# Performance work log

Hardware: AMD Instinct MI355X
Metric: run time of the kernel (lower is better)

The kernel has to match this reference:

```python
import jax, jax.numpy as jnp
import numpy as np

N_NODES = 50000
N_EDGES = 600000
N_GRAPHS = 64
HID = 128
NLAYERS = 4
IN_DIM = 5
NCLS = 5
EPS = 1e-5


def setup_inputs() -> dict:
    key = jax.random.key(0)
    ks = jax.random.split(key, 16)
    x = jax.random.normal(ks[0], (N_NODES, IN_DIM), dtype=jnp.float32)
    edge_index = jax.random.randint(ks[1], (2, N_EDGES), 0, N_NODES, dtype=jnp.int64)
    batch = jnp.sort(jax.random.randint(ks[2], (N_NODES,), 0, N_GRAPHS, dtype=jnp.int64))
    s = 0.05
    Wp = jax.random.normal(ks[3], (IN_DIM, HID), jnp.float32) * s
    bp = jnp.zeros((HID,), jnp.float32)
    Wg = jax.random.normal(ks[4], (NLAYERS, HID, HID), jnp.float32) * s
    bg = jnp.zeros((NLAYERS, HID), jnp.float32)
    gamma = jnp.ones((NLAYERS, HID), jnp.float32)
    beta = jnp.zeros((NLAYERS, HID), jnp.float32)
    W1 = jax.random.normal(ks[5], (2 * HID, HID), jnp.float32) * s
    b1 = jnp.zeros((HID,), jnp.float32)
    W2 = jax.random.normal(ks[6], (HID, HID // 2), jnp.float32) * s
    b2 = jnp.zeros((HID // 2,), jnp.float32)
    W3 = jax.random.normal(ks[7], (HID // 2, NCLS), jnp.float32) * s
    b3 = jnp.zeros((NCLS,), jnp.float32)
    return {"x": x, "edge_index": edge_index, "batch": batch, "Wp": Wp, "bp": bp,
            "Wg": Wg, "bg": bg, "gamma": gamma, "beta": beta,
            "W1": W1, "b1": b1, "W2": W2, "b2": b2, "W3": W3, "b3": b3}


def reference(x, edge_index, batch, Wp, bp, Wg, bg, gamma, beta, W1, b1, W2, b2, W3, b3):
    N = x.shape[0]
    # GCN with added self-loops and symmetric normalization (PyG GCNConv defaults)
    loop = jnp.arange(N)
    src = jnp.concatenate([edge_index[0], loop])
    dst = jnp.concatenate([edge_index[1], loop])
    deg = jax.ops.segment_sum(jnp.ones_like(dst, dtype=x.dtype), dst, num_segments=N)
    dinv = jax.lax.rsqrt(deg)  # deg >= 1 thanks to self-loops
    norm = dinv[src] * dinv[dst]  # [E+N]
    h = x @ Wp + bp  # [N, HID]
    for i in range(NLAYERS):
        m = h @ Wg[i]
        agg = jax.ops.segment_sum(m[src] * norm[:, None], dst, num_segments=N) + bg[i]
        # BatchNorm1d (training-mode stats over nodes)
        mu = jnp.mean(agg, axis=0)
        var = jnp.var(agg, axis=0)
        h = gamma[i] * (agg - mu) * jax.lax.rsqrt(var + EPS) + beta[i]
        h = jax.nn.relu(h)  # dropout is identity in eval mode
    # mean_max global pooling per graph
    cnt = jax.ops.segment_sum(jnp.ones((N,), h.dtype), batch, num_segments=N_GRAPHS)
    x_mean = jax.ops.segment_sum(h, batch, num_segments=N_GRAPHS) / jnp.maximum(cnt, 1.0)[:, None]
    x_max = jax.ops.segment_max(h, batch, num_segments=N_GRAPHS)
    x_max = jnp.where(jnp.isfinite(x_max), x_max, 0.0)
    pooled = jnp.concatenate([x_mean, x_max], axis=1)  # [B, 2*HID]
    h1 = jax.nn.relu(pooled @ W1 + b1)
    h2 = jax.nn.relu(h1 @ W2 + b2)
    return h2 @ W3 + b3  # [B, num_classes]
```

## Files before the change

### kernel.cpp

```cpp
#include <hip/hip_runtime.h>
#include <hip/hip_bf16.h>

#define N_NODES 50000
#define N_EDGES 600000
#define N_GRAPHS 64
#define HID 128
#define NLAYERS 4
#define IN_DIM 5
#define NCLS 5
#define EPS 1e-5f
#define SCAN_BLK ((N_NODES + 511) / 512)
#define POOL_CHUNKS 16
#define BSLOT 64
#define WS 136

typedef __attribute__((ext_vector_type(8))) short s16x8;
typedef __attribute__((ext_vector_type(4))) float f32x4;

__device__ __forceinline__ unsigned short f2bf(float x) {
    unsigned u = __float_as_uint(x);
    unsigned r = (u + 0x7fffu + ((u >> 16) & 1u)) >> 16;
    return (unsigned short)r;
}
__device__ __forceinline__ float2 bfpair(unsigned u) {
    float2 r;
    r.x = __uint_as_float(u << 16);
    r.y = __uint_as_float(u & 0xffff0000u);
    return r;
}
__device__ __forceinline__ float bf2f(unsigned short s) {
    return __uint_as_float(((unsigned)s) << 16);
}


__global__ void k_count(const int* __restrict__ dst, int* __restrict__ cnt) {
    int i = blockIdx.x * blockDim.x + threadIdx.x;
    if (i < N_EDGES) atomicAdd(&cnt[dst[i]], 1);
}

__global__ void k_scan1(const int* __restrict__ cnt, int* __restrict__ rp, int* __restrict__ bsum) {
    __shared__ int s[512];
    int t = threadIdx.x;
    int i = blockIdx.x * 512 + t;
    int v = (i < N_NODES) ? cnt[i] : 0;
    s[t] = v;
    __syncthreads();
    for (int off = 1; off < 512; off <<= 1) {
        int x = (t >= off) ? s[t - off] : 0;
        __syncthreads();
        s[t] += x;
        __syncthreads();
    }
    if (i < N_NODES) rp[i + 1] = s[t];
    if (t == 511) bsum[blockIdx.x] = s[511];
}

__global__ void k_scan2g(int* __restrict__ bsum, const int* __restrict__ batch,
                         int* __restrict__ gstart) {
    if (blockIdx.x == 0) {
        __shared__ int s[128];
        int t = threadIdx.x;
        int v = (t < SCAN_BLK) ? bsum[t] : 0;
        s[t] = v;
        __syncthreads();
        for (int off = 1; off < 128; off <<= 1) {
            int x = (t >= off) ? s[t - off] : 0;
            __syncthreads();
            s[t] += x;
            __syncthreads();
        }
        if (t < SCAN_BLK) bsum[t] = s[t] - v;
    } else {
        int t = threadIdx.x;
        if (t <= N_GRAPHS) {
            int lo = 0, hi = N_NODES;
            while (lo < hi) {
                int mid = (lo + hi) >> 1;
                if (batch[mid] < t) lo = mid + 1; else hi = mid;
            }
            gstart[t] = lo;
        }
    }
}

__global__ void k_scan3d(int* __restrict__ rp, const int* __restrict__ bsum,
                         const int* __restrict__ cnt, float* __restrict__ dinv) {
    int i = blockIdx.x * 512 + threadIdx.x;
    if (i < N_NODES) {
        rp[i + 1] += bsum[blockIdx.x];
        dinv[i] = rsqrtf((float)(cnt[i] + 1));
    }
    if (i == 0) rp[0] = 0;
}

__global__ void k_fill(const int* __restrict__ src, const int* __restrict__ dst,
                       const int* __restrict__ rp, int* __restrict__ cursor,
                       int2* __restrict__ cw, const float* __restrict__ dinv) {
    int e = blockIdx.x * blockDim.x + threadIdx.x;
    if (e < N_EDGES) {
        int d = dst[e];
        int pos = atomicAdd(&cursor[d], 1);
        int s = src[e];
        int2 p;
        p.x = s;
        p.y = __float_as_int(dinv[s]);
        cw[rp[d] + pos] = p;
    }
}


__global__ void k_wconv(const float* __restrict__ Wg, unsigned short* __restrict__ WtG) {
    int idx = blockIdx.x * 256 + threadIdx.x;
    if (idx < NLAYERS * HID * HID) {
        int l = idx >> 14;
        int r = idx & 16383;
        int n = r >> 7, k = r & 127;
        WtG[idx] = f2bf(Wg[l * HID * HID + k * HID + n]);
    }
}


__global__ __launch_bounds__(256) void k_gemmM(const unsigned short* __restrict__ Abf,
                                               const float* __restrict__ x,
                                               const float* __restrict__ Wp,
                                               const float* __restrict__ bp,
                                               const unsigned short* __restrict__ WtG,
                                               unsigned short* __restrict__ Bm,
                                               const float* __restrict__ psum,
                                               const float* __restrict__ psq,
                                               const float* __restrict__ gamma,
                                               const float* __restrict__ beta,
                                               int layer0) {
    __shared__ unsigned short Wt[HID * WS];
    __shared__ unsigned short Al[64 * WS];
    __shared__ float scl[HID], shf[HID];
    __shared__ float Wpl[IN_DIM * HID];
    __shared__ float bpl[HID];
    __shared__ float xl[64 * IN_DIM];
    int t = threadIdx.x;
    {
        const uint4* Wg4 = (const uint4*)WtG;
        for (int idx = t; idx < HID * 16; idx += 256) {
            int n = idx >> 4, c = idx & 15;
            *(uint4*)&Wt[n * WS + c * 8] = Wg4[idx];
        }
    }
    if (layer0) {
        for (int idx = t; idx < IN_DIM * HID; idx += 256) Wpl[idx] = Wp[idx];
        if (t < HID) bpl[t] = bp[t];
    } else if (t < HID) {
        float s = 0.f, s2 = 0.f;
#pragma unroll 8
        for (int b = 0; b < BSLOT; b++) {
            s += psum[b * HID + t];
            s2 += psq[b * HID + t];
        }
        const float invN = 1.f / (float)N_NODES;
        float mu = s * invN;
        float var = s2 * invN - mu * mu;
        float rs = rsqrtf(var + EPS) * gamma[t];
        scl[t] = rs;
        shf[t] = beta[t] - mu * rs;
    }
    int lane = t & 63, wv = t >> 6;
    int rbase = (wv & 1) * 32;
    int cbase = (wv >> 1) * 64;
    int mr = lane & 15, q = lane >> 4;
    const int numTiles = (N_NODES + 63) / 64;
    for (int tile = blockIdx.x; tile < numTiles; tile += gridDim.x) {
        int n0 = tile * 64;
        __syncthreads();
        if (layer0) {
            for (int idx = t; idx < 64 * IN_DIM; idx += 256) {
                int g = n0 * IN_DIM + idx;
                xl[idx] = (g < N_NODES * IN_DIM) ? x[g] : 0.f;
            }
            __syncthreads();
            for (int idx = t; idx < 64 * HID; idx += 256) {
                int n = idx >> 7, k = idx & 127;
                float acc = bpl[k];
#pragma unroll
                for (int j = 0; j < IN_DIM; j++) acc += xl[n * IN_DIM + j] * Wpl[j * HID + k];
                Al[n * WS + k] = f2bf(acc);
            }
        } else {
            const uint2* Ag = (const uint2*)(Abf + (size_t)n0 * HID);
            int limRow = min(64, N_NODES - n0);
            for (int idx = t; idx < 64 * 32; idx += 256) {
                int row = idx >> 5, c4 = idx & 31;
                uint2 u = (row < limRow) ? Ag[row * 32 + c4] : make_uint2(0u, 0u);
                float2 ab = bfpair(u.x);
                float2 cd = bfpair(u.y);
                int kf = c4 * 4;
                float4 sc = *(const float4*)&scl[kf];
                float4 sh = *(const float4*)&shf[kf];
                float v0 = fmaxf(ab.x * sc.x + sh.x, 0.f);
                float v1 = fmaxf(ab.y * sc.y + sh.y, 0.f);
                float v2 = fmaxf(cd.x * sc.z + sh.z, 0.f);
                float v3 = fmaxf(cd.y * sc.w + sh.w, 0.f);
                unsigned lo = (unsigned)f2bf(v0) | ((unsigned)f2bf(v1) << 16);
                unsigned hi = (unsigned)f2bf(v2) | ((unsigned)f2bf(v3) << 16);
                *(uint2*)&Al[row * WS + kf] = make_uint2(lo, hi);
            }
        }
        __syncthreads();
        f32x4 acc[2][4];
#pragma unroll
        for (int rt = 0; rt < 2; rt++)
#pragma unroll
            for (int ct = 0; ct < 4; ct++) acc[rt][ct] = (f32x4){0.f, 0.f, 0.f, 0.f};
#pragma unroll
        for (int kk = 0; kk < HID; kk += 32) {
            s16x8 a0 = *(const s16x8*)&Al[(rbase + mr) * WS + kk + q * 8];
            s16x8 a1 = *(const s16x8*)&Al[(rbase + 16 + mr) * WS + kk + q * 8];
#pragma unroll
            for (int ct = 0; ct < 4; ct++) {
                s16x8 b = *(const s16x8*)&Wt[(cbase + ct * 16 + mr) * WS + kk + q * 8];
                acc[0][ct] = __builtin_amdgcn_mfma_f32_16x16x32_bf16(a0, b, acc[0][ct], 0, 0, 0);
                acc[1][ct] = __builtin_amdgcn_mfma_f32_16x16x32_bf16(a1, b, acc[1][ct], 0, 0, 0);
            }
        }
#pragma unroll
        for (int rt = 0; rt < 2; rt++)
#pragma unroll
            for (int ct = 0; ct < 4; ct++)
#pragma unroll
                for (int r = 0; r < 4; r++) {
                    int node = n0 + rbase + rt * 16 + q * 4 + r;
                    if (node < N_NODES) {
                        int f = cbase + ct * 16 + mr;
                        Bm[(size_t)node * HID + f] = f2bf(acc[rt][ct][r]);
                    }
                }
    }
}


__global__ __launch_bounds__(256) void k_gather(const uint4* __restrict__ Bm4,
                                                const int* __restrict__ rp,
                                                const int2* __restrict__ cw,
                                                const float* __restrict__ dinv,
                                                const float* __restrict__ bg,
                                                unsigned short* __restrict__ Aout,
                                                float* __restrict__ psum,
                                                float* __restrict__ psq) {
    __shared__ float ls[4 * HID], lq[4 * HID];
    int wave = threadIdx.x >> 6;
    int lane = threadIdx.x & 63;
    int s = lane & 15;
    int p = lane >> 4;
    int f = s * 8;
    float ts0 = 0.f, ts1 = 0.f, ts2 = 0.f, ts3 = 0.f, ts4 = 0.f, ts5 = 0.f, ts6 = 0.f, ts7 = 0.f;
    float tq0 = 0.f, tq1 = 0.f, tq2 = 0.f, tq3 = 0.f, tq4 = 0.f, tq5 = 0.f, tq6 = 0.f, tq7 = 0.f;
#pragma unroll 1
    for (int it = 0; it < 4; it++) {
        int v = blockIdx.x * 16 + wave * 4 + it;
        int beg = rp[v], end = rp[v + 1];
        float dv = dinv[v];
        float a0 = 0.f, a1 = 0.f, a2 = 0.f, a3 = 0.f, a4 = 0.f, a5 = 0.f, a6 = 0.f, a7 = 0.f;
        if (p == 0) {
            uint4 u = Bm4[(size_t)v * 16 + s];
            float2 q0 = bfpair(u.x), q1 = bfpair(u.y), q2 = bfpair(u.z), q3 = bfpair(u.w);
            a0 = q0.x * dv; a1 = q0.y * dv; a2 = q1.x * dv; a3 = q1.y * dv;
            a4 = q2.x * dv; a5 = q2.y * dv; a6 = q3.x * dv; a7 = q3.y * dv;
        }
        int e = beg + p;
        for (; e + 4 < end; e += 8) {
            int2 pe0 = cw[e];
            int2 pe1 = cw[e + 4];
            uint4 u0 = Bm4[(size_t)pe0.x * 16 + s];
            uint4 u1 = Bm4[(size_t)pe1.x * 16 + s];
            float w0 = __int_as_float(pe0.y);
            float w1 = __int_as_float(pe1.y);
            float2 x0 = bfpair(u0.x), x1 = bfpair(u0.y), x2 = bfpair(u0.z), x3 = bfpair(u0.w);
            float2 y0 = bfpair(u1.x), y1 = bfpair(u1.y), y2 = bfpair(u1.z), y3 = bfpair(u1.w);
            a0 += x0.x * w0 + y0.x * w1;
            a1 += x0.y * w0 + y0.y * w1;
            a2 += x1.x * w0 + y1.x * w1;
            a3 += x1.y * w0 + y1.y * w1;
            a4 += x2.x * w0 + y2.x * w1;
            a5 += x2.y * w0 + y2.y * w1;
            a6 += x3.x * w0 + y3.x * w1;
            a7 += x3.y * w0 + y3.y * w1;
        }
        if (e < end) {
            int2 pe = cw[e];
            uint4 u = Bm4[(size_t)pe.x * 16 + s];
            float w = __int_as_float(pe.y);
            float2 x0 = bfpair(u.x), x1 = bfpair(u.y), x2 = bfpair(u.z), x3 = bfpair(u.w);
            a0 += x0.x * w; a1 += x0.y * w; a2 += x1.x * w; a3 += x1.y * w;
            a4 += x2.x * w; a5 += x2.y * w; a6 += x3.x * w; a7 += x3.y * w;
        }
        a0 += __shfl_xor(a0, 16); a1 += __shfl_xor(a1, 16);
        a2 += __shfl_xor(a2, 16); a3 += __shfl_xor(a3, 16);
        a4 += __shfl_xor(a4, 16); a5 += __shfl_xor(a5, 16);
        a6 += __shfl_xor(a6, 16); a7 += __shfl_xor(a7, 16);
        a0 += __shfl_xor(a0, 32); a1 += __shfl_xor(a1, 32);
        a2 += __shfl_xor(a2, 32); a3 += __shfl_xor(a3, 32);
        a4 += __shfl_xor(a4, 32); a5 += __shfl_xor(a5, 32);
        a6 += __shfl_xor(a6, 32); a7 += __shfl_xor(a7, 32);
        if (p == 0) {
            float r0 = a0 * dv + bg[f + 0];
            float r1 = a1 * dv + bg[f + 1];
            float r2 = a2 * dv + bg[f + 2];
            float r3 = a3 * dv + bg[f + 3];
            float r4 = a4 * dv + bg[f + 4];
            float r5 = a5 * dv + bg[f + 5];
            float r6 = a6 * dv + bg[f + 6];
            float r7 = a7 * dv + bg[f + 7];
            unsigned short b0 = f2bf(r0), b1 = f2bf(r1), b2 = f2bf(r2), b3 = f2bf(r3);
            unsigned short b4 = f2bf(r4), b5 = f2bf(r5), b6 = f2bf(r6), b7 = f2bf(r7);
            uint4 o;
            o.x = (unsigned)b0 | ((unsigned)b1 << 16);
            o.y = (unsigned)b2 | ((unsigned)b3 << 16);
            o.z = (unsigned)b4 | ((unsigned)b5 << 16);
            o.w = (unsigned)b6 | ((unsigned)b7 << 16);
            *(uint4*)&Aout[(size_t)v * HID + f] = o;
            float v0 = bf2f(b0), v1 = bf2f(b1), v2 = bf2f(b2), v3 = bf2f(b3);
            float v4 = bf2f(b4), v5 = bf2f(b5), v6 = bf2f(b6), v7 = bf2f(b7);
            ts0 += v0; ts1 += v1; ts2 += v2; ts3 += v3;
            ts4 += v4; ts5 += v5; ts6 += v6; ts7 += v7;
            tq0 += v0 * v0; tq1 += v1 * v1; tq2 += v2 * v2; tq3 += v3 * v3;
            tq4 += v4 * v4; tq5 += v5 * v5; tq6 += v6 * v6; tq7 += v7 * v7;
        }
    }
    if (p == 0) {
        float* lsw = &ls[wave * HID + f];
        float* lqw = &lq[wave * HID + f];
        lsw[0] = ts0; lsw[1] = ts1; lsw[2] = ts2; lsw[3] = ts3;
        lsw[4] = ts4; lsw[5] = ts5; lsw[6] = ts6; lsw[7] = ts7;
        lqw[0] = tq0; lqw[1] = tq1; lqw[2] = tq2; lqw[3] = tq3;
        lqw[4] = tq4; lqw[5] = tq5; lqw[6] = tq6; lqw[7] = tq7;
    }
    __syncthreads();
    int tt = threadIdx.x;
    if (tt < HID) {
        float ssum = ls[tt] + ls[HID + tt] + ls[2 * HID + tt] + ls[3 * HID + tt];
        float ssq = lq[tt] + lq[HID + tt] + lq[2 * HID + tt] + lq[3 * HID + tt];
        int slot = blockIdx.x & (BSLOT - 1);
        atomicAdd(&psum[slot * HID + tt], ssum);
        atomicAdd(&psq[slot * HID + tt], ssq);
    }
}


__global__ __launch_bounds__(128) void k_pool(const unsigned short* __restrict__ A,
                                              const float* __restrict__ psum,
                                              const float* __restrict__ psq,
                                              const float* __restrict__ gamma,
                                              const float* __restrict__ beta,
                                              const int* __restrict__ gstart,
                                              float* __restrict__ poolPart) {
    int g = blockIdx.x;
    int c = blockIdx.y;
    int f = threadIdx.x;
    float s = 0.f, s2 = 0.f;
#pragma unroll 8
    for (int b = 0; b < BSLOT; b++) {
        s += psum[b * HID + f];
        s2 += psq[b * HID + f];
    }
    const float invN = 1.f / (float)N_NODES;
    float mu = s * invN;
    float var = s2 * invN - mu * mu;
    float sc = rsqrtf(var + EPS) * gamma[f];
    float sh = beta[f] - mu * sc;
    int beg = gstart[g], end = gstart[g + 1];
    int len = end - beg;
    int per = (len + POOL_CHUNKS - 1) / POOL_CHUNKS;
    int s0 = beg + c * per;
    int s1 = min(s0 + per, end);
    float sa = 0.f, sb = 0.f, ma = 0.f, mb = 0.f;
    int n = s0;
    for (; n + 1 < s1; n += 2) {
        float v0 = bf2f(A[(size_t)n * HID + f]);
        float v1 = bf2f(A[(size_t)(n + 1) * HID + f]);
        v0 = fmaxf(v0 * sc + sh, 0.f);
        v1 = fmaxf(v1 * sc + sh, 0.f);
        sa += v0; ma = fmaxf(ma, v0);
        sb += v1; mb = fmaxf(mb, v1);
    }
    if (n < s1) {
        float v = fmaxf(bf2f(A[(size_t)n * HID + f]) * sc + sh, 0.f);
        sa += v; ma = fmaxf(ma, v);
    }
    poolPart[((size_t)g * POOL_CHUNKS + c) * 256 + f] = sa + sb;
    poolPart[((size_t)g * POOL_CHUNKS + c) * 256 + 128 + f] = fmaxf(ma, mb);
}


__global__ __launch_bounds__(128) void k_head(const float* __restrict__ poolPart,
                                              const int* __restrict__ gstart,
                                              const float* __restrict__ W1, const float* __restrict__ b1,
                                              const float* __restrict__ W2, const float* __restrict__ b2,
                                              const float* __restrict__ W3, const float* __restrict__ b3,
                                              float* __restrict__ out) {
    __shared__ float pl[2 * HID];
    __shared__ float h1[HID];
    __shared__ float h2[HID / 2];
    int g = blockIdx.x, t = threadIdx.x;
    float cnt = fmaxf((float)(gstart[g + 1] - gstart[g]), 1.f);
    float s = 0.f, mx = 0.f;
#pragma unroll
    for (int c = 0; c < POOL_CHUNKS; c++) {
        const float* p = &poolPart[((size_t)g * POOL_CHUNKS + c) * 256];
        s += p[t];
        mx = fmaxf(mx, p[128 + t]);
    }
    pl[t] = s / cnt;
    pl[HID + t] = mx;
    __syncthreads();
    float acc = b1[t];
    for (int k = 0; k < 2 * HID; k++) acc += pl[k] * W1[k * HID + t];
    h1[t] = fmaxf(acc, 0.f);
    __syncthreads();
    if (t < HID / 2) {
        float a2 = b2[t];
        for (int k = 0; k < HID; k++) a2 += h1[k] * W2[k * (HID / 2) + t];
        h2[t] = fmaxf(a2, 0.f);
    }
    __syncthreads();
    if (t < NCLS) {
        float a3 = b3[t];
        for (int k = 0; k < HID / 2; k++) a3 += h2[k] * W3[k * NCLS + t];
        out[g * NCLS + t] = a3;
    }
}

extern "C" void kernel_launch(void* const* d_in, const int* in_sizes, int n_in,
                              void* d_out, int out_size, void* d_ws, size_t ws_size,
                              hipStream_t stream) {
    const float* x     = (const float*)d_in[0];
    const int*   ei    = (const int*)d_in[1];
    const int*   batch = (const int*)d_in[2];
    const float* Wp    = (const float*)d_in[3];
    const float* bp    = (const float*)d_in[4];
    const float* Wg    = (const float*)d_in[5];
    const float* bg    = (const float*)d_in[6];
    const float* gamma = (const float*)d_in[7];
    const float* beta  = (const float*)d_in[8];
    const float* W1    = (const float*)d_in[9];
    const float* b1    = (const float*)d_in[10];
    const float* W2    = (const float*)d_in[11];
    const float* b2    = (const float*)d_in[12];
    const float* W3    = (const float*)d_in[13];
    const float* b3    = (const float*)d_in[14];
    const int* src = ei;
    const int* dst = ei + N_EDGES;
    float* out = (float*)d_out;

    char* base = (char*)d_ws;
    size_t off = 0;
    auto alloc = [&](size_t bytes) -> void* {
        void* p = base + off;
        off += (bytes + 255) & ~(size_t)255;
        return p;
    };
    int*   counts = (int*)alloc((size_t)N_NODES * 4);
    int*   cursor = (int*)alloc((size_t)N_NODES * 4);
    float* psum   = (float*)alloc((size_t)NLAYERS * BSLOT * HID * 4);
    float* psq    = (float*)alloc((size_t)NLAYERS * BSLOT * HID * 4);
    size_t zeroBytes = off;
    int*   rp      = (int*)alloc((size_t)(N_NODES + 1) * 4);
    int*   bsum    = (int*)alloc(128 * 4);
    int2*  cw      = (int2*)alloc((size_t)N_EDGES * 8);
    float* dinv    = (float*)alloc((size_t)N_NODES * 4);
    int*   gstart  = (int*)alloc((size_t)(N_GRAPHS + 1) * 4);
    float* poolPart= (float*)alloc((size_t)N_GRAPHS * POOL_CHUNKS * 256 * 4);
    unsigned short* WtG = (unsigned short*)alloc((size_t)NLAYERS * HID * HID * 2);
    unsigned short* A = (unsigned short*)alloc((size_t)N_NODES * HID * 2);
    unsigned short* B = (unsigned short*)alloc((size_t)N_NODES * HID * 2);
    (void)ws_size; (void)in_sizes; (void)n_in; (void)out_size;

    hipMemsetAsync(d_ws, 0, zeroBytes, stream);

    k_count<<<(N_EDGES + 255) / 256, 256, 0, stream>>>(dst, counts);
    k_scan1<<<SCAN_BLK, 512, 0, stream>>>(counts, rp, bsum);
    k_scan2g<<<2, 128, 0, stream>>>(bsum, batch, gstart);
    k_scan3d<<<SCAN_BLK, 512, 0, stream>>>(rp, bsum, counts, dinv);
    k_fill<<<(N_EDGES + 255) / 256, 256, 0, stream>>>(src, dst, rp, cursor, cw, dinv);
    k_wconv<<<(NLAYERS * HID * HID + 255) / 256, 256, 0, stream>>>(Wg, WtG);

    for (int i = 0; i < NLAYERS; i++) {
        int pl = (i == 0) ? 0 : (i - 1);
        k_gemmM<<<768, 256, 0, stream>>>(A, x, Wp, bp, WtG + (size_t)i * HID * HID, B,
                                         psum + (size_t)pl * BSLOT * HID,
                                         psq + (size_t)pl * BSLOT * HID,
                                         gamma + pl * HID, beta + pl * HID,
                                         (i == 0) ? 1 : 0);
        k_gather<<<N_NODES / 16, 256, 0, stream>>>((const uint4*)B, rp, cw, dinv,
                                                   bg + i * HID, A,
                                                   psum + (size_t)i * BSLOT * HID,
                                                   psq + (size_t)i * BSLOT * HID);
    }
    dim3 pg(N_GRAPHS, POOL_CHUNKS);
    k_pool<<<pg, 128, 0, stream>>>(A, psum + (size_t)3 * BSLOT * HID,
                                   psq + (size_t)3 * BSLOT * HID,
                                   gamma + 3 * HID, beta + 3 * HID, gstart, poolPart);
    k_head<<<N_GRAPHS, 128, 0, stream>>>(poolPart, gstart, W1, b1, W2, b2, W3, b3, out);
}
```

Measured before the change: 392.3 us.

## Fuse all GCN layers, pooling and head into one cooperative persistent kernel

Replaces the per-layer GEMM and gather launches, plus the pool and head kernels, with a single cooperative persistent kernel that uses grid.sync between phases. It also merges the edge fill and weight conversion into one launch. The GEMM now reads the transposed weights straight from global memory instead of staging them in LDS, so shared memory is smaller and more blocks fit per CU. This is meant to remove launch gaps and per-launch setup, at the cost of grid-wide barriers and uncached global weight loads in the MFMA loop.

New measurement: 1.050 ms. 2.68x slower.

```diff
diff --git a/kernel.cpp b/kernel.cpp
--- a/kernel.cpp
+++ b/kernel.cpp
@@ -1,5 +1,6 @@
 #include <hip/hip_runtime.h>
 #include <hip/hip_bf16.h>
+#include <hip/hip_cooperative_groups.h>
 
 #define N_NODES 50000
 #define N_EDGES 600000
@@ -10,9 +11,10 @@
 #define NCLS 5
 #define EPS 1e-5f
 #define SCAN_BLK ((N_NODES + 511) / 512)
+#define FILL_BLK ((N_EDGES + 255) / 256)
 #define POOL_CHUNKS 16
 #define BSLOT 64
-#define WS 136
+#define WS2 136
 
 typedef __attribute__((ext_vector_type(8))) short s16x8;
 typedef __attribute__((ext_vector_type(4))) float f32x4;
@@ -93,25 +95,24 @@
     if (i == 0) rp[0] = 0;
 }
 
-__global__ void k_fill(const int* __restrict__ src, const int* __restrict__ dst,
-                       const int* __restrict__ rp, int* __restrict__ cursor,
-                       int2* __restrict__ cw, const float* __restrict__ dinv) {
-    int e = blockIdx.x * blockDim.x + threadIdx.x;
-    if (e < N_EDGES) {
-        int d = dst[e];
-        int pos = atomicAdd(&cursor[d], 1);
-        int s = src[e];
-        int2 p;
-        p.x = s;
-        p.y = __float_as_int(dinv[s]);
-        cw[rp[d] + pos] = p;
-    }
-}
-
-
-__global__ void k_wconv(const float* __restrict__ Wg, unsigned short* __restrict__ WtG) {
-    int idx = blockIdx.x * 256 + threadIdx.x;
-    if (idx < NLAYERS * HID * HID) {
+__global__ void k_fillw(const int* __restrict__ src, const int* __restrict__ dst,
+                        const int* __restrict__ rp, int* __restrict__ cursor,
+                        int2* __restrict__ cw, const float* __restrict__ dinv,
+                        const float* __restrict__ Wg, unsigned short* __restrict__ WtG) {
+    int b = blockIdx.x;
+    if (b < FILL_BLK) {
+        int e = b * 256 + threadIdx.x;
+        if (e < N_EDGES) {
+            int d = dst[e];
+            int pos = atomicAdd(&cursor[d], 1);
+            int s = src[e];
+            int2 p;
+            p.x = s;
+            p.y = __float_as_int(dinv[s]);
+            cw[rp[d] + pos] = p;
+        }
+    } else {
+        int idx = (b - FILL_BLK) * 256 + threadIdx.x;
         int l = idx >> 14;
         int r = idx & 16383;
         int n = r >> 7, k = r & 127;
@@ -120,310 +121,314 @@
 }
 
 
-__global__ __launch_bounds__(256) void k_gemmM(const unsigned short* __restrict__ Abf,
-                                               const float* __restrict__ x,
-                                               const float* __restrict__ Wp,
-                                               const float* __restrict__ bp,
-                                               const unsigned short* __restrict__ WtG,
-                                               unsigned short* __restrict__ Bm,
-                                               const float* __restrict__ psum,
-                                               const float* __restrict__ psq,
-                                               const float* __restrict__ gamma,
-                                               const float* __restrict__ beta,
-                                               int layer0) {
-    __shared__ unsigned short Wt[HID * WS];
-    __shared__ unsigned short Al[64 * WS];
-    __shared__ float scl[HID], shf[HID];
-    __shared__ float Wpl[IN_DIM * HID];
-    __shared__ float bpl[HID];
-    __shared__ float xl[64 * IN_DIM];
+struct GemmSM {
+    unsigned short Al[64 * WS2];
+    union {
+        struct { float scl[HID]; float shf[HID]; } bn;
+        struct { float Wpl[IN_DIM * HID]; float bpl[HID]; } p0;
+    } u;
+};
+struct RedSM { float ls[4 * HID]; float lq[4 * HID]; };
+struct HeadSM { float pl[2 * HID]; float h1[HID]; float h2[HID / 2]; };
+union SMem { GemmSM g; RedSM r; HeadSM h; };
+
+__global__ __launch_bounds__(256) void k_mega(
+    const float* __restrict__ x,
+    const float* __restrict__ Wp, const float* __restrict__ bp,
+    const unsigned short* __restrict__ WtG,
+    const float* __restrict__ bg,
+    const float* __restrict__ gamma, const float* __restrict__ beta,
+    const int* __restrict__ rp, const int2* __restrict__ cw,
+    const float* __restrict__ dinv, const int* __restrict__ gstart,
+    const float* __restrict__ W1, const float* __restrict__ b1,
+    const float* __restrict__ W2, const float* __restrict__ b2,
+    const float* __restrict__ W3, const float* __restrict__ b3,
+    unsigned short* __restrict__ A, unsigned short* __restrict__ B,
+    float* __restrict__ psum, float* __restrict__ psq,
+    float* __restrict__ poolPart, float* __restrict__ out)
+{
+    __shared__ SMem sm;
+    cooperative_groups::grid_group grid = cooperative_groups::this_grid();
     int t = threadIdx.x;
-    {
-        const uint4* Wg4 = (const uint4*)WtG;
-        for (int idx = t; idx < HID * 16; idx += 256) {
-            int n = idx >> 4, c = idx & 15;
-            *(uint4*)&Wt[n * WS + c * 8] = Wg4[idx];
-        }
-    }
-    if (layer0) {
-        for (int idx = t; idx < IN_DIM * HID; idx += 256) Wpl[idx] = Wp[idx];
-        if (t < HID) bpl[t] = bp[t];
-    } else if (t < HID) {
-        float s = 0.f, s2 = 0.f;
-#pragma unroll 8
-        for (int b = 0; b < BSLOT; b++) {
-            s += psum[b * HID + t];
-            s2 += psq[b * HID + t];
-        }
-        const float invN = 1.f / (float)N_NODES;
-        float mu = s * invN;
-        float var = s2 * invN - mu * mu;
-        float rs = rsqrtf(var + EPS) * gamma[t];
-        scl[t] = rs;
-        shf[t] = beta[t] - mu * rs;
-    }
     int lane = t & 63, wv = t >> 6;
     int rbase = (wv & 1) * 32;
     int cbase = (wv >> 1) * 64;
     int mr = lane & 15, q = lane >> 4;
     const int numTiles = (N_NODES + 63) / 64;
-    for (int tile = blockIdx.x; tile < numTiles; tile += gridDim.x) {
-        int n0 = tile * 64;
-        __syncthreads();
-        if (layer0) {
-            for (int idx = t; idx < 64 * IN_DIM; idx += 256) {
-                int g = n0 * IN_DIM + idx;
-                xl[idx] = (g < N_NODES * IN_DIM) ? x[g] : 0.f;
-            }
+
+    for (int layer = 0; layer < NLAYERS; layer++) {
+        const unsigned short* WtL = WtG + (size_t)layer * HID * HID;
+        if (layer == 0) {
+            for (int idx = t; idx < IN_DIM * HID; idx += 256) sm.g.u.p0.Wpl[idx] = Wp[idx];
+            if (t < HID) sm.g.u.p0.bpl[t] = bp[t];
+        } else if (t < HID) {
+            const float* ps = psum + (size_t)(layer - 1) * BSLOT * HID;
+            const float* pq = psq + (size_t)(layer - 1) * BSLOT * HID;
+            float s = 0.f, s2 = 0.f;
+#pragma unroll 8
+            for (int b = 0; b < BSLOT; b++) {
+                s += ps[b * HID + t];
+                s2 += pq[b * HID + t];
+            }
+            const float invN = 1.f / (float)N_NODES;
+            float mu = s * invN;
+            float var = s2 * invN - mu * mu;
+            float rs = rsqrtf(var + EPS) * gamma[(layer - 1) * HID + t];
+            sm.g.u.bn.scl[t] = rs;
+            sm.g.u.bn.shf[t] = beta[(layer - 1) * HID + t] - mu * rs;
+        }
+        for (int tile = blockIdx.x; tile < numTiles; tile += gridDim.x) {
+            int n0 = tile * 64;
             __syncthreads();
-            for (int idx = t; idx < 64 * HID; idx += 256) {
-                int n = idx >> 7, k = idx & 127;
-                float acc = bpl[k];
-#pragma unroll
-                for (int j = 0; j < IN_DIM; j++) acc += xl[n * IN_DIM + j] * Wpl[j * HID + k];
-                Al[n * WS + k] = f2bf(acc);
-            }
-        } else {
-            const uint2* Ag = (const uint2*)(Abf + (size_t)n0 * HID);
-            int limRow = min(64, N_NODES - n0);
-            for (int idx = t; idx < 64 * 32; idx += 256) {
-                int row = idx >> 5, c4 = idx & 31;
-                uint2 u = (row < limRow) ? Ag[row * 32 + c4] : make_uint2(0u, 0u);
-                float2 ab = bfpair(u.x);
-                float2 cd = bfpair(u.y);
-                int kf = c4 * 4;
-                float4 sc = *(const float4*)&scl[kf];
-                float4 sh = *(const float4*)&shf[kf];
-                float v0 = fmaxf(ab.x * sc.x + sh.x, 0.f);
-                float v1 = fmaxf(ab.y * sc.y + sh.y, 0.f);
-                float v2 = fmaxf(cd.x * sc.z + sh.z, 0.f);
-                float v3 = fmaxf(cd.y * sc.w + sh.w, 0.f);
-                unsigned lo = (unsigned)f2bf(v0) | ((unsigned)f2bf(v1) << 16);
-                unsigned hi = (unsigned)f2bf(v2) | ((unsigned)f2bf(v3) << 16);
-                *(uint2*)&Al[row * WS + kf] = make_uint2(lo, hi);
-            }
-        }
-        __syncthreads();
-        f32x4 acc[2][4];
-#pragma unroll
-        for (int rt = 0; rt < 2; rt++)
-#pragma unroll
-            for (int ct = 0; ct < 4; ct++) acc[rt][ct] = (f32x4){0.f, 0.f, 0.f, 0.f};
-#pragma unroll
-        for (int kk = 0; kk < HID; kk += 32) {
-            s16x8 a0 = *(const s16x8*)&Al[(rbase + mr) * WS + kk + q * 8];
-            s16x8 a1 = *(const s16x8*)&Al[(rbase + 16 + mr) * WS + kk + q * 8];
-#pragma unroll
-            for (int ct = 0; ct < 4; ct++) {
-                s16x8 b = *(const s16x8*)&Wt[(cbase + ct * 16 + mr) * WS + kk + q * 8];
-                acc[0][ct] = __builtin_amdgcn_mfma_f32_16x16x32_bf16(a0, b, acc[0][ct], 0, 0, 0);
-                acc[1][ct] = __builtin_amdgcn_mfma_f32_16x16x32_bf16(a1, b, acc[1][ct], 0, 0, 0);
-            }
-        }
-#pragma unroll
-        for (int rt = 0; rt < 2; rt++)
-#pragma unroll
-            for (int ct = 0; ct < 4; ct++)
-#pragma unroll
-                for (int r = 0; r < 4; r++) {
-                    int node = n0 + rbase + rt * 16 + q * 4 + r;
+            if (layer == 0) {
+                for (int idx = t; idx < 64 * HID; idx += 256) {
+                    int n = idx >> 7, k = idx & 127;
+                    int node = n0 + n;
+                    float acc = sm.g.u.p0.bpl[k];
                     if (node < N_NODES) {
-                        int f = cbase + ct * 16 + mr;
-                        Bm[(size_t)node * HID + f] = f2bf(acc[rt][ct][r]);
-                    }
-                }
-    }
-}
-
-
-__global__ __launch_bounds__(256) void k_gather(const uint4* __restrict__ Bm4,
-                                                const int* __restrict__ rp,
-                                                const int2* __restrict__ cw,
-                                                const float* __restrict__ dinv,
-                                                const float* __restrict__ bg,
-                                                unsigned short* __restrict__ Aout,
-                                                float* __restrict__ psum,
-                                                float* __restrict__ psq) {
-    __shared__ float ls[4 * HID], lq[4 * HID];
-    int wave = threadIdx.x >> 6;
-    int lane = threadIdx.x & 63;
-    int s = lane & 15;
-    int p = lane >> 4;
-    int f = s * 8;
-    float ts0 = 0.f, ts1 = 0.f, ts2 = 0.f, ts3 = 0.f, ts4 = 0.f, ts5 = 0.f, ts6 = 0.f, ts7 = 0.f;
-    float tq0 = 0.f, tq1 = 0.f, tq2 = 0.f, tq3 = 0.f, tq4 = 0.f, tq5 = 0.f, tq6 = 0.f, tq7 = 0.f;
+#pragma unroll
+                        for (int j = 0; j < IN_DIM; j++)
+                            acc += x[node * IN_DIM + j] * sm.g.u.p0.Wpl[j * HID + k];
+                    }
+                    sm.g.Al[n * WS2 + k] = f2bf(acc);
+                }
+            } else {
+                const uint2* Ag = (const uint2*)(A + (size_t)n0 * HID);
+                int limRow = min(64, N_NODES - n0);
+                for (int idx = t; idx < 64 * 32; idx += 256) {
+                    int row = idx >> 5, c4 = idx & 31;
+                    uint2 u = (row < limRow) ? Ag[row * 32 + c4] : make_uint2(0u, 0u);
+                    float2 ab = bfpair(u.x);
+                    float2 cd = bfpair(u.y);
+                    int kf = c4 * 4;
+                    float4 sc = *(const float4*)&sm.g.u.bn.scl[kf];
+                    float4 sh = *(const float4*)&sm.g.u.bn.shf[kf];
+                    float v0 = fmaxf(ab.x * sc.x + sh.x, 0.f);
+                    float v1 = fmaxf(ab.y * sc.y + sh.y, 0.f);
+                    float v2 = fmaxf(cd.x * sc.z + sh.z, 0.f);
+                    float v3 = fmaxf(cd.y * sc.w + sh.w, 0.f);
+                    unsigned lo = (unsigned)f2bf(v0) | ((unsigned)f2bf(v1) << 16);
+                    unsigned hi = (unsigned)f2bf(v2) | ((unsigned)f2bf(v3) << 16);
+                    *(uint2*)&sm.g.Al[row * WS2 + kf] = make_uint2(lo, hi);
+                }
+            }
+            __syncthreads();
+            f32x4 acc[2][4];
+#pragma unroll
+            for (int rt = 0; rt < 2; rt++)
+#pragma unroll
+                for (int ct = 0; ct < 4; ct++) acc[rt][ct] = (f32x4){0.f, 0.f, 0.f, 0.f};
+#pragma unroll
+            for (int kk = 0; kk < HID; kk += 32) {
+                s16x8 a0 = *(const s16x8*)&sm.g.Al[(rbase + mr) * WS2 + kk + q * 8];
+                s16x8 a1 = *(const s16x8*)&sm.g.Al[(rbase + 16 + mr) * WS2 + kk + q * 8];
+#pragma unroll
+                for (int ct = 0; ct < 4; ct++) {
+                    s16x8 b = *(const s16x8*)&WtL[(cbase + ct * 16 + mr) * HID + kk + q * 8];
+                    acc[0][ct] = __builtin_amdgcn_mfma_f32_16x16x32_bf16(a0, b, acc[0][ct], 0, 0, 0);
+                    acc[1][ct] = __builtin_amdgcn_mfma_f32_16x16x32_bf16(a1, b, acc[1][ct], 0, 0, 0);
+                }
+            }
+#pragma unroll
+            for (int rt = 0; rt < 2; rt++)
+#pragma unroll
+                for (int ct = 0; ct < 4; ct++)
+#pragma unroll
+                    for (int r = 0; r < 4; r++) {
+                        int node = n0 + rbase + rt * 16 + q * 4 + r;
+                        if (node < N_NODES) {
+                            int f = cbase + ct * 16 + mr;
+                            B[(size_t)node * HID + f] = f2bf(acc[rt][ct][r]);
+                        }
+                    }
+        }
+        grid.sync();
+
+        {
+            const uint4* Bm4 = (const uint4*)B;
+            const float* bgL = bg + layer * HID;
+            float* psL = psum + (size_t)layer * BSLOT * HID;
+            float* pqL = psq + (size_t)layer * BSLOT * HID;
+            int s = lane & 15;
+            int p = lane >> 4;
+            int f = s * 8;
+            for (int grp = blockIdx.x; grp < N_NODES / 16; grp += gridDim.x) {
+                float ts0 = 0.f, ts1 = 0.f, ts2 = 0.f, ts3 = 0.f;
+                float ts4 = 0.f, ts5 = 0.f, ts6 = 0.f, ts7 = 0.f;
+                float tq0 = 0.f, tq1 = 0.f, tq2 = 0.f, tq3 = 0.f;
+                float tq4 = 0.f, tq5 = 0.f, tq6 = 0.f, tq7 = 0.f;
 #pragma unroll 1
-    for (int it = 0; it < 4; it++) {
-        int v = blockIdx.x * 16 + wave * 4 + it;
-        int beg = rp[v], end = rp[v + 1];
-        float dv = dinv[v];
-        float a0 = 0.f, a1 = 0.f, a2 = 0.f, a3 = 0.f, a4 = 0.f, a5 = 0.f, a6 = 0.f, a7 = 0.f;
-        if (p == 0) {
-            uint4 u = Bm4[(size_t)v * 16 + s];
-            float2 q0 = bfpair(u.x), q1 = bfpair(u.y), q2 = bfpair(u.z), q3 = bfpair(u.w);
-            a0 = q0.x * dv; a1 = q0.y * dv; a2 = q1.x * dv; a3 = q1.y * dv;
-            a4 = q2.x * dv; a5 = q2.y * dv; a6 = q3.x * dv; a7 = q3.y * dv;
-        }
-        int e = beg + p;
-        for (; e + 4 < end; e += 8) {
-            int2 pe0 = cw[e];
-            int2 pe1 = cw[e + 4];
-            uint4 u0 = Bm4[(size_t)pe0.x * 16 + s];
-            uint4 u1 = Bm4[(size_t)pe1.x * 16 + s];
-            float w0 = __int_as_float(pe0.y);
-            float w1 = __int_as_float(pe1.y);
-            float2 x0 = bfpair(u0.x), x1 = bfpair(u0.y), x2 = bfpair(u0.z), x3 = bfpair(u0.w);
-            float2 y0 = bfpair(u1.x), y1 = bfpair(u1.y), y2 = bfpair(u1.z), y3 = bfpair(u1.w);
-            a0 += x0.x * w0 + y0.x * w1;
-            a1 += x0.y * w0 + y0.y * w1;
-            a2 += x1.x * w0 + y1.x * w1;
-            a3 += x1.y * w0 + y1.y * w1;
-            a4 += x2.x * w0 + y2.x * w1;
-            a5 += x2.y * w0 + y2.y * w1;
-            a6 += x3.x * w0 + y3.x * w1;
-            a7 += x3.y * w0 + y3.y * w1;
-        }
-        if (e < end) {
-            int2 pe = cw[e];
-            uint4 u = Bm4[(size_t)pe.x * 16 + s];
-            float w = __int_as_float(pe.y);
-            float2 x0 = bfpair(u.x), x1 = bfpair(u.y), x2 = bfpair(u.z), x3 = bfpair(u.w);
-            a0 += x0.x * w; a1 += x0.y * w; a2 += x1.x * w; a3 += x1.y * w;
-            a4 += x2.x * w; a5 += x2.y * w; a6 += x3.x * w; a7 += x3.y * w;
-        }
-        a0 += __shfl_xor(a0, 16); a1 += __shfl_xor(a1, 16);
-        a2 += __shfl_xor(a2, 16); a3 += __shfl_xor(a3, 16);
-        a4 += __shfl_xor(a4, 16); a5 += __shfl_xor(a5, 16);
-        a6 += __shfl_xor(a6, 16); a7 += __shfl_xor(a7, 16);
-        a0 += __shfl_xor(a0, 32); a1 += __shfl_xor(a1, 32);
-        a2 += __shfl_xor(a2, 32); a3 += __shfl_xor(a3, 32);
-        a4 += __shfl_xor(a4, 32); a5 += __shfl_xor(a5, 32);
-        a6 += __shfl_xor(a6, 32); a7 += __shfl_xor(a7, 32);
-        if (p == 0) {
-            float r0 = a0 * dv + bg[f + 0];
-            float r1 = a1 * dv + bg[f + 1];
-            float r2 = a2 * dv + bg[f + 2];
-            float r3 = a3 * dv + bg[f + 3];
-            float r4 = a4 * dv + bg[f + 4];
-            float r5 = a5 * dv + bg[f + 5];
-            float r6 = a6 * dv + bg[f + 6];
-            float r7 = a7 * dv + bg[f + 7];
-            unsigned short b0 = f2bf(r0), b1 = f2bf(r1), b2 = f2bf(r2), b3 = f2bf(r3);
-            unsigned short b4 = f2bf(r4), b5 = f2bf(r5), b6 = f2bf(r6), b7 = f2bf(r7);
-            uint4 o;
-            o.x = (unsigned)b0 | ((unsigned)b1 << 16);
-            o.y = (unsigned)b2 | ((unsigned)b3 << 16);
-            o.z = (unsigned)b4 | ((unsigned)b5 << 16);
-            o.w = (unsigned)b6 | ((unsigned)b7 << 16);
-            *(uint4*)&Aout[(size_t)v * HID + f] = o;
-            float v0 = bf2f(b0), v1 = bf2f(b1), v2 = bf2f(b2), v3 = bf2f(b3);
-            float v4 = bf2f(b4), v5 = bf2f(b5), v6 = bf2f(b6), v7 = bf2f(b7);
-            ts0 += v0; ts1 += v1; ts2 += v2; ts3 += v3;
-            ts4 += v4; ts5 += v5; ts6 += v6; ts7 += v7;
-            tq0 += v0 * v0; tq1 += v1 * v1; tq2 += v2 * v2; tq3 += v3 * v3;
-            tq4 += v4 * v4; tq5 += v5 * v5; tq6 += v6 * v6; tq7 += v7 * v7;
-        }
-    }
-    if (p == 0) {
-        float* lsw = &ls[wave * HID + f];
-        float* lqw = &lq[wave * HID + f];
-        lsw[0] = ts0; lsw[1] = ts1; lsw[2] = ts2; lsw[3] = ts3;
-        lsw[4] = ts4; lsw[5] = ts5; lsw[6] = ts6; lsw[7] = ts7;
-        lqw[0] = tq0; lqw[1] = tq1; lqw[2] = tq2; lqw[3] = tq3;
-        lqw[4] = tq4; lqw[5] = tq5; lqw[6] = tq6; lqw[7] = tq7;
-    }
-    __syncthreads();
-    int tt = threadIdx.x;
-    if (tt < HID) {
-        float ssum = ls[tt] + ls[HID + tt] + ls[2 * HID + tt] + ls[3 * HID + tt];
-        float ssq = lq[tt] + lq[HID + tt] + lq[2 * HID + tt] + lq[3 * HID + tt];
-        int slot = blockIdx.x & (BSLOT - 1);
-        atomicAdd(&psum[slot * HID + tt], ssum);
-        atomicAdd(&psq[slot * HID + tt], ssq);
-    }
-}
-
-
-__global__ __launch_bounds__(128) void k_pool(const unsigned short* __restrict__ A,
-                                              const float* __restrict__ psum,
-                                              const float* __restrict__ psq,
-                                              const float* __restrict__ gamma,
-                                              const float* __restrict__ beta,
-                                              const int* __restrict__ gstart,
-                                              float* __restrict__ poolPart) {
-    int g = blockIdx.x;
-    int c = blockIdx.y;
-    int f = threadIdx.x;
-    float s = 0.f, s2 = 0.f;
+                for (int it = 0; it < 4; it++) {
+                    int v = grp * 16 + wv * 4 + it;
+                    int beg = rp[v], end = rp[v + 1];
+                    float dv = dinv[v];
+                    float a0 = 0.f, a1 = 0.f, a2 = 0.f, a3 = 0.f;
+                    float a4 = 0.f, a5 = 0.f, a6 = 0.f, a7 = 0.f;
+                    if (p == 0) {
+                        uint4 u = Bm4[(size_t)v * 16 + s];
+                        float2 q0 = bfpair(u.x), q1 = bfpair(u.y), q2 = bfpair(u.z), q3 = bfpair(u.w);
+                        a0 = q0.x * dv; a1 = q0.y * dv; a2 = q1.x * dv; a3 = q1.y * dv;
+                        a4 = q2.x * dv; a5 = q2.y * dv; a6 = q3.x * dv; a7 = q3.y * dv;
+                    }
+                    int e = beg + p;
+                    for (; e + 4 < end; e += 8) {
+                        int2 pe0 = cw[e];
+                        int2 pe1 = cw[e + 4];
+                        uint4 u0 = Bm4[(size_t)pe0.x * 16 + s];
+                        uint4 u1 = Bm4[(size_t)pe1.x * 16 + s];
+                        float w0 = __int_as_float(pe0.y);
+                        float w1 = __int_as_float(pe1.y);
+                        float2 x0 = bfpair(u0.x), x1 = bfpair(u0.y), x2 = bfpair(u0.z), x3 = bfpair(u0.w);
+                        float2 y0 = bfpair(u1.x), y1 = bfpair(u1.y), y2 = bfpair(u1.z), y3 = bfpair(u1.w);
+                        a0 += x0.x * w0 + y0.x * w1;
+                        a1 += x0.y * w0 + y0.y * w1;
+                        a2 += x1.x * w0 + y1.x * w1;
+                        a3 += x1.y * w0 + y1.y * w1;
+                        a4 += x2.x * w0 + y2.x * w1;
+                        a5 += x2.y * w0 + y2.y * w1;
+                        a6 += x3.x * w0 + y3.x * w1;
+                        a7 += x3.y * w0 + y3.y * w1;
+                    }
+                    if (e < end) {
+                        int2 pe = cw[e];
+                        uint4 u = Bm4[(size_t)pe.x * 16 + s];
+                        float w = __int_as_float(pe.y);
+                        float2 x0 = bfpair(u.x), x1 = bfpair(u.y), x2 = bfpair(u.z), x3 = bfpair(u.w);
+                        a0 += x0.x * w; a1 += x0.y * w; a2 += x1.x * w; a3 += x1.y * w;
+                        a4 += x2.x * w; a5 += x2.y * w; a6 += x3.x * w; a7 += x3.y * w;
+                    }
+                    a0 += __shfl_xor(a0, 16); a1 += __shfl_xor(a1, 16);
+                    a2 += __shfl_xor(a2, 16); a3 += __shfl_xor(a3, 16);
+                    a4 += __shfl_xor(a4, 16); a5 += __shfl_xor(a5, 16);
+                    a6 += __shfl_xor(a6, 16); a7 += __shfl_xor(a7, 16);
+                    a0 += __shfl_xor(a0, 32); a1 += __shfl_xor(a1, 32);
+                    a2 += __shfl_xor(a2, 32); a3 += __shfl_xor(a3, 32);
+                    a4 += __shfl_xor(a4, 32); a5 += __shfl_xor(a5, 32);
+                    a6 += __shfl_xor(a6, 32); a7 += __shfl_xor(a7, 32);
+                    if (p == 0) {
+                        float r0 = a0 * dv + bgL[f + 0];
+                        float r1 = a1 * dv + bgL[f + 1];
+                        float r2 = a2 * dv + bgL[f + 2];
+                        float r3 = a3 * dv + bgL[f + 3];
+                        float r4 = a4 * dv + bgL[f + 4];
+                        float r5 = a5 * dv + bgL[f + 5];
+                        float r6 = a6 * dv + bgL[f + 6];
+                        float r7 = a7 * dv + bgL[f + 7];
+                        unsigned short b0 = f2bf(r0), b1 = f2bf(r1), b2 = f2bf(r2), b3 = f2bf(r3);
+                        unsigned short b4 = f2bf(r4), b5 = f2bf(r5), b6 = f2bf(r6), b7 = f2bf(r7);
+                        uint4 o;
+                        o.x = (unsigned)b0 | ((unsigned)b1 << 16);
+                        o.y = (unsigned)b2 | ((unsigned)b3 << 16);
+                        o.z = (unsigned)b4 | ((unsigned)b5 << 16);
+                        o.w = (unsigned)b6 | ((unsigned)b7 << 16);
+                        *(uint4*)&A[(size_t)v * HID + f] = o;
+                        float v0 = bf2f(b0), v1 = bf2f(b1), v2 = bf2f(b2), v3 = bf2f(b3);
+                        float v4 = bf2f(b4), v5 = bf2f(b5), v6 = bf2f(b6), v7 = bf2f(b7);
+                        ts0 += v0; ts1 += v1; ts2 += v2; ts3 += v3;
+                        ts4 += v4; ts5 += v5; ts6 += v6; ts7 += v7;
+                        tq0 += v0 * v0; tq1 += v1 * v1; tq2 += v2 * v2; tq3 += v3 * v3;
+                        tq4 += v4 * v4; tq5 += v5 * v5; tq6 += v6 * v6; tq7 += v7 * v7;
+                    }
+                }
+                if (p == 0) {
+                    float* lsw = &sm.r.ls[wv * HID + f];
+                    float* lqw = &sm.r.lq[wv * HID + f];
+                    lsw[0] = ts0; lsw[1] = ts1; lsw[2] = ts2; lsw[3] = ts3;
+                    lsw[4] = ts4; lsw[5] = ts5; lsw[6] = ts6; lsw[7] = ts7;
+                    lqw[0] = tq0; lqw[1] = tq1; lqw[2] = tq2; lqw[3] = tq3;
+                    lqw[4] = tq4; lqw[5] = tq5; lqw[6] = tq6; lqw[7] = tq7;
+                }
+                __syncthreads();
+                if (t < HID) {
+                    float ssum = sm.r.ls[t] + sm.r.ls[HID + t] + sm.r.ls[2 * HID + t] + sm.r.ls[3 * HID + t];
+                    float ssq = sm.r.lq[t] + sm.r.lq[HID + t] + sm.r.lq[2 * HID + t] + sm.r.lq[3 * HID + t];
+                    int slot = grp & (BSLOT - 1);
+                    atomicAdd(&psL[slot * HID + t], ssum);
+                    atomicAdd(&pqL[slot * HID + t], ssq);
+                }
+                __syncthreads();
+            }
+        }
+        grid.sync();
+    }
+
+    {
+        int f = t & 127;
+        int half = t >> 7;
+        if (blockIdx.x * 2 < N_GRAPHS * POOL_CHUNKS) {
+            const float* ps = psum + (size_t)(NLAYERS - 1) * BSLOT * HID;
+            const float* pq = psq + (size_t)(NLAYERS - 1) * BSLOT * HID;
+            float s = 0.f, s2 = 0.f;
 #pragma unroll 8
-    for (int b = 0; b < BSLOT; b++) {
-        s += psum[b * HID + f];
-        s2 += psq[b * HID + f];
-    }
-    const float invN = 1.f / (float)N_NODES;
-    float mu = s * invN;
-    float var = s2 * invN - mu * mu;
-    float sc = rsqrtf(var + EPS) * gamma[f];
-    float sh = beta[f] - mu * sc;
-    int beg = gstart[g], end = gstart[g + 1];
-    int len = end - beg;
-    int per = (len + POOL_CHUNKS - 1) / POOL_CHUNKS;
-    int s0 = beg + c * per;
-    int s1 = min(s0 + per, end);
-    float sa = 0.f, sb = 0.f, ma = 0.f, mb = 0.f;
-    int n = s0;
-    for (; n + 1 < s1; n += 2) {
-        float v0 = bf2f(A[(size_t)n * HID + f]);
-        float v1 = bf2f(A[(size_t)(n + 1) * HID + f]);
-        v0 = fmaxf(v0 * sc + sh, 0.f);
-        v1 = fmaxf(v1 * sc + sh, 0.f);
-        sa += v0; ma = fmaxf(ma, v0);
-        sb += v1; mb = fmaxf(mb, v1);
-    }
-    if (n < s1) {
-        float v = fmaxf(bf2f(A[(size_t)n * HID + f]) * sc + sh, 0.f);
-        sa += v; ma = fmaxf(ma, v);
-    }
-    poolPart[((size_t)g * POOL_CHUNKS + c) * 256 + f] = sa + sb;
-    poolPart[((size_t)g * POOL_CHUNKS + c) * 256 + 128 + f] = fmaxf(ma, mb);
-}
-
-
-__global__ __launch_bounds__(128) void k_head(const float* __restrict__ poolPart,
-                                              const int* __restrict__ gstart,
-                                              const float* __restrict__ W1, const float* __restrict__ b1,
-                                              const float* __restrict__ W2, const float* __restrict__ b2,
-                                              const float* __restrict__ W3, const float* __restrict__ b3,
-                                              float* __restrict__ out) {
-    __shared__ float pl[2 * HID];
-    __shared__ float h1[HID];
-    __shared__ float h2[HID / 2];
-    int g = blockIdx.x, t = threadIdx.x;
-    float cnt = fmaxf((float)(gstart[g + 1] - gstart[g]), 1.f);
-    float s = 0.f, mx = 0.f;
-#pragma unroll
-    for (int c = 0; c < POOL_CHUNKS; c++) {
-        const float* p = &poolPart[((size_t)g * POOL_CHUNKS + c) * 256];
-        s += p[t];
-        mx = fmaxf(mx, p[128 + t]);
-    }
-    pl[t] = s / cnt;
-    pl[HID + t] = mx;
-    __syncthreads();
-    float acc = b1[t];
-    for (int k = 0; k < 2 * HID; k++) acc += pl[k] * W1[k * HID + t];
-    h1[t] = fmaxf(acc, 0.f);
-    __syncthreads();
-    if (t < HID / 2) {
-        float a2 = b2[t];
-        for (int k = 0; k < HID; k++) a2 += h1[k] * W2[k * (HID / 2) + t];
-        h2[t] = fmaxf(a2, 0.f);
-    }
-    __syncthreads();
-    if (t < NCLS) {
-        float a3 = b3[t];
-        for (int k = 0; k < HID / 2; k++) a3 += h2[k] * W3[k * NCLS + t];
-        out[g * NCLS + t] = a3;
+            for (int b = 0; b < BSLOT; b++) {
+                s += ps[b * HID + f];
+                s2 += pq[b * HID + f];
+            }
+            const float invN = 1.f / (float)N_NODES;
+            float mu = s * invN;
+            float var = s2 * invN - mu * mu;
+            float sc = rsqrtf(var + EPS) * gamma[(NLAYERS - 1) * HID + f];
+            float sh = beta[(NLAYERS - 1) * HID + f] - mu * sc;
+            for (int item = blockIdx.x * 2 + half; item < N_GRAPHS * POOL_CHUNKS; item += gridDim.x * 2) {
+                int g = item >> 4, c = item & 15;
+                int beg = gstart[g], end = gstart[g + 1];
+                int len = end - beg;
+                int per = (len + POOL_CHUNKS - 1) / POOL_CHUNKS;
+                int s0 = beg + c * per;
+                int s1 = min(s0 + per, end);
+                float sa = 0.f, sb = 0.f, ma = 0.f, mb = 0.f;
+                int n = s0;
+                for (; n + 1 < s1; n += 2) {
+                    float v0 = bf2f(A[(size_t)n * HID + f]);
+                    float v1 = bf2f(A[(size_t)(n + 1) * HID + f]);
+                    v0 = fmaxf(v0 * sc + sh, 0.f);
+                    v1 = fmaxf(v1 * sc + sh, 0.f);
+                    sa += v0; ma = fmaxf(ma, v0);
+                    sb += v1; mb = fmaxf(mb, v1);
+                }
+                if (n < s1) {
+                    float v = fmaxf(bf2f(A[(size_t)n * HID + f]) * sc + sh, 0.f);
+                    sa += v; ma = fmaxf(ma, v);
+                }
+                poolPart[(size_t)item * 256 + f] = sa + sb;
+                poolPart[(size_t)item * 256 + 128 + f] = fmaxf(ma, mb);
+            }
+        }
+    }
+    grid.sync();
+
+    if (blockIdx.x < N_GRAPHS) {
+        int g = blockIdx.x;
+        if (t < HID) {
+            float cnt = fmaxf((float)(gstart[g + 1] - gstart[g]), 1.f);
+            float s = 0.f, mx = 0.f;
+#pragma unroll
+            for (int c = 0; c < POOL_CHUNKS; c++) {
+                const float* p = &poolPart[(size_t)(g * POOL_CHUNKS + c) * 256];
+                s += p[t];
+                mx = fmaxf(mx, p[128 + t]);
+            }
+            sm.h.pl[t] = s / cnt;
+            sm.h.pl[HID + t] = mx;
+        }
+        __syncthreads();
+        if (t < HID) {
+            float acc = b1[t];
+            for (int k = 0; k < 2 * HID; k++) acc += sm.h.pl[k] * W1[k * HID + t];
+            sm.h.h1[t] = fmaxf(acc, 0.f);
+        }
+        __syncthreads();
+        if (t < HID / 2) {
+            float a2 = b2[t];
+            for (int k = 0; k < HID; k++) a2 += sm.h.h1[k] * W2[k * (HID / 2) + t];
+            sm.h.h2[t] = fmaxf(a2, 0.f);
+        }
+        __syncthreads();
+        if (t < NCLS) {
+            float a3 = b3[t];
+            for (int k = 0; k < HID / 2; k++) a3 += sm.h.h2[k] * W3[k * NCLS + t];
+            out[g * NCLS + t] = a3;
+        }
     }
 }
 
@@ -478,24 +483,17 @@
     k_scan1<<<SCAN_BLK, 512, 0, stream>>>(counts, rp, bsum);
     k_scan2g<<<2, 128, 0, stream>>>(bsum, batch, gstart);
     k_scan3d<<<SCAN_BLK, 512, 0, stream>>>(rp, bsum, counts, dinv);
-    k_fill<<<(N_EDGES + 255) / 256, 256, 0, stream>>>(src, dst, rp, cursor, cw, dinv);
-    k_wconv<<<(NLAYERS * HID * HID + 255) / 256, 256, 0, stream>>>(Wg, WtG);
-
-    for (int i = 0; i < NLAYERS; i++) {
-        int pl = (i == 0) ? 0 : (i - 1);
-        k_gemmM<<<768, 256, 0, stream>>>(A, x, Wp, bp, WtG + (size_t)i * HID * HID, B,
-                                         psum + (size_t)pl * BSLOT * HID,
-                                         psq + (size_t)pl * BSLOT * HID,
-                                         gamma + pl * HID, beta + pl * HID,
-                                         (i == 0) ? 1 : 0);
-        k_gather<<<N_NODES / 16, 256, 0, stream>>>((const uint4*)B, rp, cw, dinv,
-                                                   bg + i * HID, A,
-                                                   psum + (size_t)i * BSLOT * HID,
-                                                   psq + (size_t)i * BSLOT * HID);
-    }
-    dim3 pg(N_GRAPHS, POOL_CHUNKS);
-    k_pool<<<pg, 128, 0, stream>>>(A, psum + (size_t)3 * BSLOT * HID,
-                                   psq + (size_t)3 * BSLOT * HID,
-                                   gamma + 3 * HID, beta + 3 * HID, gstart, poolPart);
-    k_head<<<N_GRAPHS, 128, 0, stream>>>(poolPart, gstart, W1, b1, W2, b2, W3, b3, out);
-}
+    k_fillw<<<FILL_BLK + (NLAYERS * HID * HID) / 256, 256, 0, stream>>>(
+        src, dst, rp, cursor, cw, dinv, Wg, WtG);
+
+    int nb = 0;
+    if (hipOccupancyMaxActiveBlocksPerMultiprocessor(&nb, k_mega, 256, 0) != hipSuccess || nb < 1)
+        nb = 2;
+    int gridSz = nb * 256;
+    void* args[] = {(void*)&x, (void*)&Wp, (void*)&bp, (void*)&WtG, (void*)&bg,
+                    (void*)&gamma, (void*)&beta, (void*)&rp, (void*)&cw, (void*)&dinv,
+                    (void*)&gstart, (void*)&W1, (void*)&b1, (void*)&W2, (void*)&b2,
+                    (void*)&W3, (void*)&b3, (void*)&A, (void*)&B, (void*)&psum,
+                    (void*)&psq, (void*)&poolPart, (void*)&out};
+    hipLaunchCooperativeKernel((void*)k_mega, dim3(gridSz), dim3(256), args, 0, stream);
+}
```
